# Kernel optimization log

Hardware: AMD Instinct MI355X
Metric: run time of the kernel (lower is better)

Reference implementation:

```python
import jax, jax.numpy as jnp
import numpy as np

E, K, CAP = 64, 8, 512  # num_experts, top_k, per-expert capacity (>= max tokens routed, T*K/E=256 expected)


def setup_inputs() -> dict:
    key = jax.random.key(0)
    ks = jax.random.split(key, 10)
    B, N, D, H, BT, O = 4, 512, 768, 2048, 256, 768
    def w(k, shape, fan_in):
        return jax.random.normal(k, shape, jnp.float32) * np.float32(1.0 / np.sqrt(fan_in))
    return {
        "x": jax.random.normal(ks[0], (B, N, D), jnp.float32),
        "noise": jax.random.normal(ks[1], (B, N, E), jnp.float32),
        "Wr": w(ks[2], (D, E), D), "br": jnp.zeros((E,), jnp.float32),
        "Wn": w(ks[3], (D, E), D), "bn": jnp.zeros((E,), jnp.float32),
        "W1": w(ks[4], (E, D, H), D), "b1": jnp.zeros((E, H), jnp.float32),
        "W2": w(ks[5], (E, H, H), H), "b2": jnp.zeros((E, H), jnp.float32),
        "W3": w(ks[6], (E, H, BT), H), "b3": jnp.zeros((E, BT), jnp.float32),
        "Wo": w(ks[7], (E, BT, O), BT), "bo": jnp.zeros((E, O), jnp.float32),
        "ln_w": jnp.ones((O,), jnp.float32), "ln_b": jnp.zeros((O,), jnp.float32),
    }


def reference(x, noise, Wr, br, Wn, bn, W1, b1, W2, b2, W3, b3, Wo, bo, ln_w, ln_b):
    B, N, D = x.shape
    O = Wo.shape[-1]
    T = B * N
    # --- noisy top-k router ---
    logits = x @ Wr + br                                   # [B,N,E]
    noisy = logits + noise * jax.nn.softplus(x @ Wn + bn)  # [B,N,E]
    topv, topi = jax.lax.top_k(noisy, K)                   # [B,N,K]
    gk = jax.nn.softmax(topv, axis=-1)                     # softmax over top-k == softmax with -inf elsewhere
    fx = x.reshape(T, D)
    fi = topi.reshape(T, K)
    fg = gk.reshape(T, K)
    gate = jnp.zeros((T, E), x.dtype).at[jnp.arange(T)[:, None], fi].set(fg)  # [T,E], zero off top-k
    sel = gate > 0                                         # [T,E] token->expert assignment mask
    # --- capacity-based dispatch (exact: CAP >> max tokens per expert) ---
    selT = sel.T                                           # [E,T]
    idx = jnp.argsort(jnp.logical_not(selT), axis=-1)[:, :CAP]   # [E,CAP] selected tokens first (stable)
    valid = jnp.take_along_axis(selT, idx, axis=1)               # [E,CAP]
    g = jnp.take_along_axis(gate.T, idx, axis=1) * valid          # [E,CAP]
    xin = fx[idx]                                                  # [E,CAP,D]
    gelu = lambda t: jax.nn.gelu(t, approximate=False)
    h = gelu(jnp.einsum('ecd,edh->ech', xin, W1) + b1[:, None, :])
    h = gelu(jnp.einsum('ech,ehf->ecf', h, W2) + b2[:, None, :])
    h = jnp.einsum('ecf,efb->ecb', h, W3) + b3[:, None, :]
    y = jnp.einsum('ecb,ebo->eco', h, Wo) + bo[:, None, :]         # [E,CAP,O]
    y = y * g[:, :, None]                                          # invalid slots weighted by 0
    out = jnp.zeros((T, O), x.dtype).at[idx].add(y)                # scatter-add combine
    # --- LayerNorm ---
    mu = out.mean(-1, keepdims=True)
    var = out.var(-1, keepdims=True)
    out = (out - mu) / jnp.sqrt(var + 1e-5) * ln_w + ln_b
    return out.reshape(B, N, O)
```

## Files before the change

kernel.cpp:

```cpp
#include <hip/hip_runtime.h>
#include <math.h>

#define T_TOK 2048
#define NE 64
#define KTOP 8
#define CAPC 512
#define DIN 768
#define HD 2048
#define BTD 256
#define OD 768

typedef short bf16x8 __attribute__((ext_vector_type(8)));
typedef float f32x4 __attribute__((ext_vector_type(4)));

__device__ __forceinline__ unsigned short f2bf(float f) {
  unsigned u = __float_as_uint(f);
  u += 0x7FFF + ((u >> 16) & 1);
  return (unsigned short)(u >> 16);
}
__device__ __forceinline__ unsigned cvt2(float a, float b) {
  unsigned r;
  asm("v_cvt_pk_bf16_f32 %0, %1, %2" : "=v"(r) : "v"(a), "v"(b));
  return r;
}
__device__ __forceinline__ float gelu_exact(float v) {
  return 0.5f * v * (1.0f + erff(v * 0.7071067811865476f));
}
__device__ __forceinline__ void glds16(unsigned short* lds, const unsigned short* g) {
  __builtin_amdgcn_global_load_lds(
      (const __attribute__((address_space(1))) void*)g,
      (__attribute__((address_space(3))) void*)lds, 16, 0, 0);
}

__global__ __launch_bounds__(256) void cvt_x(const float* __restrict__ x,
                                             unsigned short* __restrict__ xb) {
  int i = blockIdx.x * 256 + threadIdx.x;
  float4 v = ((const float4*)x)[i];
  ushort4 o;
  o.x = f2bf(v.x); o.y = f2bf(v.y); o.z = f2bf(v.z); o.w = f2bf(v.w);
  ((ushort4*)xb)[i] = o;
}

__global__ __launch_bounds__(256) void router_kernel(
    const float* __restrict__ x, const float* __restrict__ noise,
    const float* __restrict__ Wr, const float* __restrict__ br,
    const float* __restrict__ Wn, const float* __restrict__ bn,
    float* __restrict__ gate, int* __restrict__ slotm)
{
  __shared__ float xs[8][DIN];
  __shared__ float wrs[64][NE];
  __shared__ float wns[64][NE];
  const int tid = threadIdx.x;
  const int t0 = blockIdx.x * 8;
  for (int i = tid; i < 8 * (DIN / 4); i += 256) {
    int tt = i / (DIN / 4), c = i % (DIN / 4);
    ((float4*)xs[tt])[c] = ((const float4*)(x + (size_t)(t0 + tt) * DIN))[c];
  }
  const int lane = tid & 63;
  const int wv = tid >> 6;
  const int e = lane;
  const int ta = 2 * wv, tb = ta + 1;
  float ar0 = br[e], ar1 = ar0, an0 = bn[e], an1 = an0;
  for (int d0 = 0; d0 < DIN; d0 += 64) {
    __syncthreads();
    for (int i = tid; i < 64 * NE / 4; i += 256) {
      int dd = i >> 4, c4 = (i & 15) * 4;
      *(float4*)&wrs[dd][c4] = *(const float4*)&Wr[(size_t)(d0 + dd) * NE + c4];
      *(float4*)&wns[dd][c4] = *(const float4*)&Wn[(size_t)(d0 + dd) * NE + c4];
    }
    __syncthreads();
    #pragma unroll 8
    for (int dd = 0; dd < 64; dd++) {
      float wr = wrs[dd][e], wn = wns[dd][e];
      float xa = xs[ta][d0 + dd], xb = xs[tb][d0 + dd];
      ar0 = fmaf(xa, wr, ar0); ar1 = fmaf(xb, wr, ar1);
      an0 = fmaf(xa, wn, an0); an1 = fmaf(xb, wn, an1);
    }
  }
  #pragma unroll
  for (int s = 0; s < 2; s++) {
    int t = t0 + ta + s;
    float lr = s ? ar1 : ar0;
    float lnv = s ? an1 : an0;
    float sp = fmaxf(lnv, 0.f) + log1pf(expf(-fabsf(lnv)));
    float v = lr + noise[(size_t)t * NE + e] * sp;
    float cur = v;
    float topv[KTOP]; int topi[KTOP];
    #pragma unroll
    for (int j = 0; j < KTOP; j++) {
      float bv = cur; int bi = e;
      #pragma unroll
      for (int off = 32; off > 0; off >>= 1) {
        float ov = __shfl_xor(bv, off);
        int   oi = __shfl_xor(bi, off);
        if (ov > bv || (ov == bv && oi < bi)) { bv = ov; bi = oi; }
      }
      topv[j] = bv; topi[j] = bi;
      if (e == bi) cur = -INFINITY;
    }
    float mx = topv[0], se = 0.f, pv[KTOP];
    #pragma unroll
    for (int j = 0; j < KTOP; j++) { pv[j] = expf(topv[j] - mx); se += pv[j]; }
    float inv = 1.f / se;
    float g = 0.f; int sl = -1;
    #pragma unroll
    for (int j = 0; j < KTOP; j++) if (topi[j] == e) { g = pv[j] * inv; sl = j; }
    gate[(size_t)t * NE + e] = (sl >= 0) ? g : 0.f;
    slotm[(size_t)t * NE + e] = sl;
  }
}

__global__ __launch_bounds__(256) void dispatch_kernel(
    const float* __restrict__ gate, const int* __restrict__ slotm,
    int* __restrict__ tok_idx, float* __restrict__ tok_g,
    int* __restrict__ tok_slot, int* __restrict__ counts)
{
  const int e = blockIdx.x;
  const int tid = threadIdx.x;
  __shared__ int wave_off[4];
  int base = 0;
  for (int t0 = 0; t0 < T_TOK; t0 += 256) {
    int t = t0 + tid;
    float g = gate[(size_t)t * NE + e];
    bool p = g > 0.f;
    unsigned long long m = __ballot(p);
    int wv = tid >> 6, lane = tid & 63;
    int pre = __popcll(m & ((1ull << lane) - 1ull));
    if (lane == 0) wave_off[wv] = __popcll(m);
    __syncthreads();
    int off = 0;
    for (int w = 0; w < wv; w++) off += wave_off[w];
    int tot = wave_off[0] + wave_off[1] + wave_off[2] + wave_off[3];
    if (p) {
      int pos = base + off + pre;
      if (pos < CAPC) {
        tok_idx[(size_t)e * CAPC + pos] = t;
        tok_g[(size_t)e * CAPC + pos] = g;
        tok_slot[(size_t)e * CAPC + pos] = slotm[(size_t)t * NE + e];
      }
    }
    base += tot;
    __syncthreads();
  }
  if (tid == 0) counts[e] = min(base, CAPC);
}

template<int KD, int NDT, bool AGATHER, int EPI, int NBN, int BPE>
__global__ __launch_bounds__(512, 1) void moe_gemm320(
    const unsigned short* __restrict__ Abf, const float* __restrict__ Bw,
    const float* __restrict__ bias, void* __restrict__ Outp,
    const int* __restrict__ tok_idx, const float* __restrict__ tok_g,
    const int* __restrict__ tok_slot, const int* __restrict__ counts)
{
  constexpr int NK = KD / 32;
  static_assert(NK % 4 == 0 && NK >= 8, "NK must be multiple of 4");
  const int bid = blockIdx.x;
  const int xcd = bid & 7;
  const int q   = bid >> 3;
  const int e     = (q / BPE) * 8 + xcd;
  const int inner = q % BPE;
  const int n0 = (inner % NBN) * 128;
  const int m0 = (inner / NBN) * 320;
  const int cnt = counts[e];
  if (m0 >= cnt) return;
  const int tid = threadIdx.x;
  const int lane = tid & 63, wave = tid >> 6;

  __shared__ unsigned short AL[3][320][32];
  __shared__ unsigned short BL[2][128][40];

  const bool isB = wave < 4;
  const int  w4  = wave & 3;

  const float* bp = Bw + (size_t)e * KD * NDT + (size_t)(8 * w4) * NDT + n0 + 2 * lane;
  float2 breg[4][8];

  size_t a_off[5];
  if (!isB) {
    #pragma unroll
    for (int qq = 0; qq < 5; qq++) {
      int r  = w4 * 80 + qq * 16 + (lane >> 2);
      int cq = ((lane & 3) - (r >> 1)) & 3;
      size_t rowb;
      if (AGATHER) {
        int gr = min(m0 + r, CAPC - 1);
        int tk = (gr < cnt) ? tok_idx[(size_t)e * CAPC + gr] : 0;
        rowb = (size_t)tk * KD;
      } else {
        int gr = min(m0 + r, CAPC - 1);
        rowb = ((size_t)e * CAPC + gr) * KD;
      }
      a_off[qq] = rowb + 8 * cq;
    }
  }

  auto stageA = [&](int t, unsigned short* Abuf) {
    #pragma unroll
    for (int qq = 0; qq < 5; qq++)
      glds16(Abuf + w4 * 2560 + qq * 512, Abf + a_off[qq] + (size_t)t * 32);
  };
  auto loadB = [&](int t, int p) {
    const float* pb = bp + (size_t)t * 32 * NDT;
    #pragma unroll
    for (int j = 0; j < 8; j++) breg[p][j] = *(const float2*)(pb + (size_t)j * NDT);
  };
  auto writeB = [&](unsigned short* Bbuf, int p) {
    uint4 rx, ry;
    rx.x = cvt2(breg[p][0].x, breg[p][1].x); rx.y = cvt2(breg[p][2].x, breg[p][3].x);
    rx.z = cvt2(breg[p][4].x, breg[p][5].x); rx.w = cvt2(breg[p][6].x, breg[p][7].x);
    ry.x = cvt2(breg[p][0].y, breg[p][1].y); ry.y = cvt2(breg[p][2].y, breg[p][3].y);
    ry.z = cvt2(breg[p][4].y, breg[p][5].y); ry.w = cvt2(breg[p][6].y, breg[p][7].y);
    *(uint4*)(Bbuf + (2 * lane) * 40 + 8 * w4)     = rx;
    *(uint4*)(Bbuf + (2 * lane + 1) * 40 + 8 * w4) = ry;
  };

  const int wm = (wave >> 1) * 80;
  const int wn = (wave & 1) * 64;
  const int li = lane & 15, lg = lane >> 4;
  const int kxa = 8 * ((lg + ((li >> 1) & 3)) & 3);

  f32x4 acc[5][4];
  #pragma unroll
  for (int i = 0; i < 5; i++)
    #pragma unroll
    for (int j = 0; j < 4; j++) acc[i][j] = (f32x4){0.f, 0.f, 0.f, 0.f};

  auto step = [&](const unsigned short* Abuf, const unsigned short* Bbuf) {
    bf16x8 afr[5], bfr[4];
    #pragma unroll
    for (int mi = 0; mi < 5; mi++)
      afr[mi] = *(const bf16x8*)(Abuf + (wm + mi * 16 + li) * 32 + kxa);
    #pragma unroll
    for (int ni = 0; ni < 4; ni++)
      bfr[ni] = *(const bf16x8*)(Bbuf + (wn + ni * 16 + li) * 40 + lg * 8);
    __builtin_amdgcn_s_setprio(1);
    #pragma unroll
    for (int mi = 0; mi < 5; mi++)
      #pragma unroll
      for (int ni = 0; ni < 4; ni++)
        acc[mi][ni] = __builtin_amdgcn_mfma_f32_16x16x32_bf16(afr[mi], bfr[ni], acc[mi][ni], 0, 0, 0);
    __builtin_amdgcn_s_setprio(0);
  };

  unsigned short *A0 = &AL[0][0][0], *A1 = &AL[1][0][0], *A2 = &AL[2][0][0];
  unsigned short *B0 = &BL[0][0][0], *B1 = &BL[1][0][0];

  if (isB) {
    loadB(0, 0); loadB(1, 1); loadB(2, 2);
    asm volatile("s_waitcnt vmcnt(16)" ::: "memory");
    writeB(B0, 0);
    asm volatile("s_waitcnt lgkmcnt(0)" ::: "memory");
  } else {
    stageA(0, A0); stageA(1, A1);
    asm volatile("s_waitcnt vmcnt(5)" ::: "memory");
  }
  __builtin_amdgcn_s_barrier();

  #define SUBITER(p)                                                        \
    do {                                                                    \
      const int jj = jb + (p);                                              \
      if (isB) loadB(min(jj + 3, NK - 1), ((p) + 3) & 3);                   \
      else     stageA(min(jj + 2, NK - 1), A2);                             \
      step(A0, B0);                                                         \
      if (isB) {                                                            \
        asm volatile("s_waitcnt vmcnt(16)" ::: "memory");                   \
        writeB(B1, ((p) + 1) & 3);                                          \
        asm volatile("s_waitcnt lgkmcnt(0)" ::: "memory");                  \
      } else {                                                              \
        asm volatile("s_waitcnt vmcnt(5)" ::: "memory");                    \
      }                                                                     \
      __builtin_amdgcn_s_barrier();                                         \
      unsigned short* ta = A0; A0 = A1; A1 = A2; A2 = ta;                   \
      unsigned short* tb = B0; B0 = B1; B1 = tb;                            \
    } while (0)

  for (int jb = 0; jb < NK; jb += 4) {
    SUBITER(0); SUBITER(1); SUBITER(2); SUBITER(3);
  }
  #undef SUBITER
  asm volatile("s_waitcnt vmcnt(0)" ::: "memory");

  const float* bpb = bias + (size_t)e * NDT;
  #pragma unroll
  for (int mi = 0; mi < 5; mi++) {
    #pragma unroll
    for (int ni = 0; ni < 4; ni++) {
      const int ncol = n0 + wn + ni * 16 + li;
      const float bb = bpb[ncol];
      #pragma unroll
      for (int qq = 0; qq < 4; qq++) {
        const int r = wm + mi * 16 + lg * 4 + qq;
        const int gr = m0 + r;
        if (gr < cnt) {
          float v = acc[mi][ni][qq] + bb;
          if (EPI == 0) v = gelu_exact(v);
          ((unsigned short*)Outp)[((size_t)e * CAPC + gr) * NDT + ncol] = f2bf(v);
        }
      }
    }
  }
}

template<int KD, int ND, bool AGATHER, int EPI, int NBN, int BPE>
__global__ __launch_bounds__(256, 2) void moe_gemm(
    const unsigned short* __restrict__ Abf, const float* __restrict__ Bw,
    const float* __restrict__ bias, void* __restrict__ Outp,
    const int* __restrict__ tok_idx, const float* __restrict__ tok_g,
    const int* __restrict__ tok_slot, const int* __restrict__ counts)
{
  constexpr int NK = KD / 32;
  static_assert(NK % 4 == 0 && NK >= 8, "NK must be multiple of 4");
  const int bid = blockIdx.x;
  const int xcd = bid & 7;
  const int q   = bid >> 3;
  const int e     = (q / BPE) * 8 + xcd;
  const int inner = q % BPE;
  const int n0 = (inner % NBN) * 128;
  const int m0 = (inner / NBN) * 128;
  const int cnt = counts[e];
  if (m0 >= cnt) return;
  const int tid = threadIdx.x;

  __shared__ unsigned short AL[4][128][32];
  __shared__ unsigned short BL[4][128][40];
  __shared__ int   s_tok[128];
  __shared__ float s_g[128];
  __shared__ int   s_slot[128];

  if (EPI == 2 && tid < 128) {
    int gr = m0 + tid;
    if (gr < cnt) {
      s_tok[tid]  = tok_idx[(size_t)e * CAPC + gr];
      s_g[tid]    = tok_g[(size_t)e * CAPC + gr];
      s_slot[tid] = tok_slot[(size_t)e * CAPC + gr];
    }
  }

  const int ar0 = tid >> 2;
  const int ac  = 8 * (((tid & 3) - (tid >> 3)) & 3);
  size_t arow0, arow1;
  if (AGATHER) {
    int g0 = m0 + ar0, g1 = m0 + 64 + ar0;
    int t0i = (g0 < cnt) ? tok_idx[(size_t)e * CAPC + g0] : 0;
    int t1i = (g1 < cnt) ? tok_idx[(size_t)e * CAPC + g1] : 0;
    arow0 = (size_t)t0i * KD; arow1 = (size_t)t1i * KD;
  } else {
    arow0 = ((size_t)e * CAPC + m0 + ar0) * KD;
    arow1 = arow0 + (size_t)64 * KD;
  }
  const unsigned short* ap0 = Abf + arow0 + ac;
  const unsigned short* ap1 = Abf + arow1 + ac;
  const int awb = (tid & 192) * 8;

  const int l = tid & 63, w = tid >> 6;
  const float* bp = Bw + (size_t)e * KD * ND + (size_t)(8 * w) * ND + n0 + 2 * l;

  float2 breg[4][8];

  auto stageA = [&](int t, int s) {
    glds16(&AL[s][0][0] + awb,        ap0 + t * 32);
    glds16(&AL[s][0][0] + 2048 + awb, ap1 + t * 32);
  };
  auto loadB = [&](int t, int p) {
    const float* pb = bp + (size_t)t * 32 * ND;
    #pragma unroll
    for (int j = 0; j < 8; j++) breg[p][j] = *(const float2*)(pb + (size_t)j * ND);
  };
  auto writeB = [&](int s, int p) {
    uint4 rx, ry;
    rx.x = cvt2(breg[p][0].x, breg[p][1].x); rx.y = cvt2(breg[p][2].x, breg[p][3].x);
    rx.z = cvt2(breg[p][4].x, breg[p][5].x); rx.w = cvt2(breg[p][6].x, breg[p][7].x);
    ry.x = cvt2(breg[p][0].y, breg[p][1].y); ry.y = cvt2(breg[p][2].y, breg[p][3].y);
    ry.z = cvt2(breg[p][4].y, breg[p][5].y); ry.w = cvt2(breg[p][6].y, breg[p][7].y);
    *(uint4*)&BL[s][2 * l][8 * w]     = rx;
    *(uint4*)&BL[s][2 * l + 1][8 * w] = ry;
  };

  const int lane = tid & 63, wv = tid >> 6;
  const int wm = (wv >> 1) * 64, wn = (wv & 1) * 64;
  const int li = lane & 15, lg = lane >> 4;
  const int kxa = 8 * ((lg + ((li >> 1) & 3)) & 3);

  f32x4 acc[4][4];
  #pragma unroll
  for (int i = 0; i < 4; i++)
    #pragma unroll
    for (int j = 0; j < 4; j++) acc[i][j] = (f32x4){0.f, 0.f, 0.f, 0.f};

  auto step = [&](int s) {
    bf16x8 afr[4], bfr[4];
    #pragma unroll
    for (int mi = 0; mi < 4; mi++)
      afr[mi] = *(const bf16x8*)&AL[s][wm + mi * 16 + li][kxa];
    #pragma unroll
    for (int ni = 0; ni < 4; ni++)
      bfr[ni] = *(const bf16x8*)&BL[s][wn + ni * 16 + li][lg * 8];
    __builtin_amdgcn_s_setprio(1);
    #pragma unroll
    for (int mi = 0; mi < 4; mi++)
      #pragma unroll
      for (int ni = 0; ni < 4; ni++)
        acc[mi][ni] = __builtin_amdgcn_mfma_f32_16x16x32_bf16(afr[mi], bfr[ni], acc[mi][ni], 0, 0, 0);
    __builtin_amdgcn_s_setprio(0);
  };

  loadB(0, 0);
  stageA(0, 0); loadB(1, 1);
  stageA(1, 1); loadB(2, 2);
  stageA(2, 2); loadB(3, 3);
  asm volatile("s_waitcnt vmcnt(28)" ::: "memory");
  writeB(0, 0);
  asm volatile("s_waitcnt lgkmcnt(0)" ::: "memory");
  __builtin_amdgcn_s_barrier();

  #define SUBITER(p)                                                        \
    do {                                                                    \
      const int jj = jb + (p);                                              \
      stageA(min(jj + 3, NK - 1), ((p) + 3) & 3);                           \
      loadB(min(jj + 4, NK - 1), (p));                                      \
      step(p);                                                              \
      asm volatile("s_waitcnt vmcnt(28)" ::: "memory");                     \
      writeB(((p) + 1) & 3, ((p) + 1) & 3);                                 \
      asm volatile("s_waitcnt lgkmcnt(0)" ::: "memory");                    \
      __builtin_amdgcn_s_barrier();                                         \
    } while (0)

  for (int jb = 0; jb < NK; jb += 4) {
    SUBITER(0); SUBITER(1); SUBITER(2); SUBITER(3);
  }
  #undef SUBITER
  asm volatile("s_waitcnt vmcnt(0)" ::: "memory");

  const float* bpb = bias + (size_t)e * ND;
  #pragma unroll
  for (int mi = 0; mi < 4; mi++) {
    #pragma unroll
    for (int ni = 0; ni < 4; ni++) {
      const int ncol = n0 + wn + ni * 16 + li;
      const float bb = bpb[ncol];
      #pragma unroll
      for (int qq = 0; qq < 4; qq++) {
        const int r = wm + mi * 16 + lg * 4 + qq;
        const int gr = m0 + r;
        if (gr < cnt) {
          float v = acc[mi][ni][qq] + bb;
          if (EPI == 0) {
            v = gelu_exact(v);
            ((unsigned short*)Outp)[((size_t)e * CAPC + gr) * ND + ncol] = f2bf(v);
          } else if (EPI == 1) {
            ((unsigned short*)Outp)[((size_t)e * CAPC + gr) * ND + ncol] = f2bf(v);
          } else {
            ((float*)Outp)[((size_t)s_tok[r] * KTOP + s_slot[r]) * OD + ncol] = v * s_g[r];
          }
        }
      }
    }
  }
}

__global__ __launch_bounds__(256) void combine_ln(
    const float* __restrict__ yd, const float* __restrict__ lw,
    const float* __restrict__ lb, float* __restrict__ out)
{
  const int t = blockIdx.x, tid = threadIdx.x;
  float v[3];
  #pragma unroll
  for (int i = 0; i < 3; i++) {
    const int c = tid + 256 * i;
    float s = 0.f;
    #pragma unroll
    for (int j = 0; j < KTOP; j++) s += yd[((size_t)t * KTOP + j) * OD + c];
    v[i] = s;
  }
  float s1 = v[0] + v[1] + v[2];
  float s2 = v[0] * v[0] + v[1] * v[1] + v[2] * v[2];
  #pragma unroll
  for (int off = 32; off > 0; off >>= 1) {
    s1 += __shfl_xor(s1, off);
    s2 += __shfl_xor(s2, off);
  }
  __shared__ float as1[4], as2[4];
  const int lane = tid & 63, wv = tid >> 6;
  if (lane == 0) { as1[wv] = s1; as2[wv] = s2; }
  __syncthreads();
  s1 = as1[0] + as1[1] + as1[2] + as1[3];
  s2 = as2[0] + as2[1] + as2[2] + as2[3];
  const float mu = s1 * (1.f / OD);
  const float var = s2 * (1.f / OD) - mu * mu;
  const float rstd = rsqrtf(var + 1e-5f);
  #pragma unroll
  for (int i = 0; i < 3; i++) {
    const int c = tid + 256 * i;
    out[(size_t)t * OD + c] = (v[i] - mu) * rstd * lw[c] + lb[c];
  }
}

extern "C" void kernel_launch(void* const* d_in, const int* in_sizes, int n_in,
                              void* d_out, int out_size, void* d_ws, size_t ws_size,
                              hipStream_t stream) {
  const float* x     = (const float*)d_in[0];
  const float* noise = (const float*)d_in[1];
  const float* Wr    = (const float*)d_in[2];
  const float* br    = (const float*)d_in[3];
  const float* Wn    = (const float*)d_in[4];
  const float* bn    = (const float*)d_in[5];
  const float* W1    = (const float*)d_in[6];
  const float* b1    = (const float*)d_in[7];
  const float* W2    = (const float*)d_in[8];
  const float* b2    = (const float*)d_in[9];
  const float* W3    = (const float*)d_in[10];
  const float* b3    = (const float*)d_in[11];
  const float* Wo    = (const float*)d_in[12];
  const float* bo    = (const float*)d_in[13];
  const float* lw    = (const float*)d_in[14];
  const float* lb    = (const float*)d_in[15];
  float* out = (float*)d_out;

  char* ws = (char*)d_ws;
  constexpr size_t OFF_GATE = 0;
  constexpr size_t OFF_SLOT = OFF_GATE + (size_t)T_TOK * NE * 4;
  constexpr size_t OFF_TIDX = OFF_SLOT + (size_t)T_TOK * NE * 4;
  constexpr size_t OFF_TG   = OFF_TIDX + (size_t)NE * CAPC * 4;
  constexpr size_t OFF_TSL  = OFF_TG + (size_t)NE * CAPC * 4;
  constexpr size_t OFF_CNT  = OFF_TSL + (size_t)NE * CAPC * 4;
  constexpr size_t OFF_YD   = ((OFF_CNT + NE * 4) + 255) & ~(size_t)255;
  constexpr size_t SZ_YD    = (size_t)T_TOK * KTOP * OD * 4;
  constexpr size_t OFF_H1   = OFF_YD + SZ_YD;
  constexpr size_t OFF_H2   = OFF_H1 + (size_t)NE * CAPC * HD * 2;
  constexpr size_t OFF_H3   = OFF_H2 + (size_t)NE * CAPC * HD * 2;
  constexpr size_t OFF_XBF  = OFF_H3 + (size_t)NE * CAPC * BTD * 2;

  float* gate = (float*)(ws + OFF_GATE);
  int*   slot = (int*)(ws + OFF_SLOT);
  int*   tidx = (int*)(ws + OFF_TIDX);
  float* tg   = (float*)(ws + OFF_TG);
  int*   tsl  = (int*)(ws + OFF_TSL);
  int*   cnts = (int*)(ws + OFF_CNT);
  float* yd   = (float*)(ws + OFF_YD);
  unsigned short* h1  = (unsigned short*)(ws + OFF_H1);
  unsigned short* h2  = (unsigned short*)(ws + OFF_H2);
  unsigned short* h3  = (unsigned short*)(ws + OFF_H3);
  unsigned short* xbf = (unsigned short*)(ws + OFF_XBF);

  hipMemsetAsync(yd, 0, SZ_YD, stream);
  cvt_x<<<T_TOK * DIN / 4 / 256, 256, 0, stream>>>(x, xbf);
  router_kernel<<<T_TOK / 8, 256, 0, stream>>>(x, noise, Wr, br, Wn, bn, gate, slot);
  dispatch_kernel<<<NE, 256, 0, stream>>>(gate, slot, tidx, tg, tsl, cnts);
  moe_gemm320<DIN, HD, true, 0, 16, 32><<<2048, 512, 0, stream>>>(
      xbf, W1, b1, h1, tidx, tg, tsl, cnts);
  moe_gemm320<HD, HD, false, 0, 16, 32><<<2048, 512, 0, stream>>>(
      h1, W2, b2, h2, tidx, tg, tsl, cnts);
  moe_gemm320<HD, BTD, false, 1, 2, 4><<<256, 512, 0, stream>>>(
      h2, W3, b3, h3, tidx, tg, tsl, cnts);
  moe_gemm<BTD, OD, false, 2, 6, 24><<<1536, 256, 0, stream>>>(
      h3, Wo, bo, yd, tidx, tg, tsl, cnts);
  combine_ln<<<T_TOK, 256, 0, stream>>>(yd, lw, lb, out);
}
```

Before: 845.7 us.

## Split-K the W3 GEMM, swizzle B LDS layout, store combine buffer in bf16

The small W3 GEMM (N=256) launched only 256 blocks, so it now runs as a 2-way split-K writing fp32 partials, and a new h3sum kernel adds the partials and bias and converts to bf16. The B tile in LDS gets an XOR swizzle on its k-chunk to cut bank conflicts in the write and fragment reads. The per-slot output buffer yd is stored as bf16 instead of fp32, halving the memset, scatter and combine traffic at some cost in precision. Split-K adds an extra kernel launch plus an fp32 partial round trip through memory.

Measured after the change: 814.2 us. 3.7% less time.

```diff
diff --git a/kernel.cpp b/kernel.cpp
--- a/kernel.cpp
+++ b/kernel.cpp
@@ -145,22 +145,25 @@
   if (tid == 0) counts[e] = min(base, CAPC);
 }
 
-template<int KD, int NDT, bool AGATHER, int EPI, int NBN, int BPE>
+template<int KD, int NDT, bool AGATHER, int EPI, int NBN, int BPE, int KSPL>
 __global__ __launch_bounds__(512, 1) void moe_gemm320(
     const unsigned short* __restrict__ Abf, const float* __restrict__ Bw,
     const float* __restrict__ bias, void* __restrict__ Outp,
     const int* __restrict__ tok_idx, const float* __restrict__ tok_g,
     const int* __restrict__ tok_slot, const int* __restrict__ counts)
 {
-  constexpr int NK = KD / 32;
-  static_assert(NK % 4 == 0 && NK >= 8, "NK must be multiple of 4");
+  constexpr int NKT = KD / 32;
+  constexpr int NKL = NKT / KSPL;
+  static_assert(NKL % 4 == 0 && NKL >= 8, "NKL must be multiple of 4");
   const int bid = blockIdx.x;
   const int xcd = bid & 7;
   const int q   = bid >> 3;
   const int e     = (q / BPE) * 8 + xcd;
   const int inner = q % BPE;
-  const int n0 = (inner % NBN) * 128;
-  const int m0 = (inner / NBN) * 320;
+  const int n0  = (inner % NBN) * 128;
+  const int ksp = (inner / NBN) % KSPL;
+  const int m0  = (inner / (NBN * KSPL)) * 320;
+  const int kbase = ksp * (KD / KSPL);
   const int cnt = counts[e];
   if (m0 >= cnt) return;
   const int tid = threadIdx.x;
@@ -172,8 +175,9 @@
   const bool isB = wave < 4;
   const int  w4  = wave & 3;
 
-  const float* bp = Bw + (size_t)e * KD * NDT + (size_t)(8 * w4) * NDT + n0 + 2 * lane;
+  const float* bp = Bw + (size_t)e * KD * NDT + (size_t)(kbase + 8 * w4) * NDT + n0 + 2 * lane;
   float2 breg[4][8];
+  const int bxs = 8 * (w4 ^ ((lane >> 2) & 3));
 
   size_t a_off[5];
   if (!isB) {
@@ -182,15 +186,14 @@
       int r  = w4 * 80 + qq * 16 + (lane >> 2);
       int cq = ((lane & 3) - (r >> 1)) & 3;
       size_t rowb;
+      int gr = min(m0 + r, CAPC - 1);
       if (AGATHER) {
-        int gr = min(m0 + r, CAPC - 1);
         int tk = (gr < cnt) ? tok_idx[(size_t)e * CAPC + gr] : 0;
         rowb = (size_t)tk * KD;
       } else {
-        int gr = min(m0 + r, CAPC - 1);
         rowb = ((size_t)e * CAPC + gr) * KD;
       }
-      a_off[qq] = rowb + 8 * cq;
+      a_off[qq] = rowb + kbase + 8 * cq;
     }
   }
 
@@ -210,14 +213,20 @@
     rx.z = cvt2(breg[p][4].x, breg[p][5].x); rx.w = cvt2(breg[p][6].x, breg[p][7].x);
     ry.x = cvt2(breg[p][0].y, breg[p][1].y); ry.y = cvt2(breg[p][2].y, breg[p][3].y);
     ry.z = cvt2(breg[p][4].y, breg[p][5].y); ry.w = cvt2(breg[p][6].y, breg[p][7].y);
-    *(uint4*)(Bbuf + (2 * lane) * 40 + 8 * w4)     = rx;
-    *(uint4*)(Bbuf + (2 * lane + 1) * 40 + 8 * w4) = ry;
+    *(uint4*)(Bbuf + (2 * lane) * 40 + bxs)     = rx;
+    *(uint4*)(Bbuf + (2 * lane + 1) * 40 + bxs) = ry;
   };
 
   const int wm = (wave >> 1) * 80;
   const int wn = (wave & 1) * 64;
   const int li = lane & 15, lg = lane >> 4;
   const int kxa = 8 * ((lg + ((li >> 1) & 3)) & 3);
+  int kxb[4];
+  #pragma unroll
+  for (int ni = 0; ni < 4; ni++) {
+    int row = wn + ni * 16 + li;
+    kxb[ni] = row * 40 + 8 * (lg ^ ((row >> 3) & 3));
+  }
 
   f32x4 acc[5][4];
   #pragma unroll
@@ -232,7 +241,7 @@
       afr[mi] = *(const bf16x8*)(Abuf + (wm + mi * 16 + li) * 32 + kxa);
     #pragma unroll
     for (int ni = 0; ni < 4; ni++)
-      bfr[ni] = *(const bf16x8*)(Bbuf + (wn + ni * 16 + li) * 40 + lg * 8);
+      bfr[ni] = *(const bf16x8*)(Bbuf + kxb[ni]);
     __builtin_amdgcn_s_setprio(1);
     #pragma unroll
     for (int mi = 0; mi < 5; mi++)
@@ -259,8 +268,8 @@
   #define SUBITER(p)                                                        \
     do {                                                                    \
       const int jj = jb + (p);                                              \
-      if (isB) loadB(min(jj + 3, NK - 1), ((p) + 3) & 3);                   \
-      else     stageA(min(jj + 2, NK - 1), A2);                             \
+      if (isB) loadB(min(jj + 3, NKL - 1), ((p) + 3) & 3);                  \
+      else     stageA(min(jj + 2, NKL - 1), A2);                            \
       step(A0, B0);                                                         \
       if (isB) {                                                            \
         asm volatile("s_waitcnt vmcnt(16)" ::: "memory");                   \
@@ -274,7 +283,7 @@
       unsigned short* tb = B0; B0 = B1; B1 = tb;                            \
     } while (0)
 
-  for (int jb = 0; jb < NK; jb += 4) {
+  for (int jb = 0; jb < NKL; jb += 4) {
     SUBITER(0); SUBITER(1); SUBITER(2); SUBITER(3);
   }
   #undef SUBITER
@@ -286,19 +295,41 @@
     #pragma unroll
     for (int ni = 0; ni < 4; ni++) {
       const int ncol = n0 + wn + ni * 16 + li;
-      const float bb = bpb[ncol];
+      const float bb = (EPI == 3) ? 0.f : bpb[ncol];
       #pragma unroll
       for (int qq = 0; qq < 4; qq++) {
         const int r = wm + mi * 16 + lg * 4 + qq;
         const int gr = m0 + r;
         if (gr < cnt) {
           float v = acc[mi][ni][qq] + bb;
-          if (EPI == 0) v = gelu_exact(v);
-          ((unsigned short*)Outp)[((size_t)e * CAPC + gr) * NDT + ncol] = f2bf(v);
+          if (EPI == 0) {
+            v = gelu_exact(v);
+            ((unsigned short*)Outp)[((size_t)e * CAPC + gr) * NDT + ncol] = f2bf(v);
+          } else if (EPI == 1) {
+            ((unsigned short*)Outp)[((size_t)e * CAPC + gr) * NDT + ncol] = f2bf(v);
+          } else {
+            ((float*)Outp)[((size_t)ksp * NE * CAPC + (size_t)e * CAPC + gr) * NDT + ncol] = v;
+          }
         }
       }
     }
   }
+}
+
+__global__ __launch_bounds__(256) void h3sum(const float* __restrict__ p,
+                                             const float* __restrict__ b3,
+                                             unsigned short* __restrict__ h3) {
+  constexpr size_t SEG = (size_t)NE * CAPC * BTD;
+  size_t i = (size_t)blockIdx.x * 1024 + (size_t)threadIdx.x * 4;
+  float4 a = *(const float4*)(p + i);
+  float4 b = *(const float4*)(p + SEG + i);
+  int c = (int)(i % BTD);
+  int e = (int)(i / ((size_t)CAPC * BTD));
+  const float* bb = b3 + (size_t)e * BTD + c;
+  ushort4 o;
+  o.x = f2bf(a.x + b.x + bb[0]); o.y = f2bf(a.y + b.y + bb[1]);
+  o.z = f2bf(a.z + b.z + bb[2]); o.w = f2bf(a.w + b.w + bb[3]);
+  *(ushort4*)(h3 + i) = o;
 }
 
 template<int KD, int ND, bool AGATHER, int EPI, int NBN, int BPE>
@@ -450,7 +481,8 @@
           } else if (EPI == 1) {
             ((unsigned short*)Outp)[((size_t)e * CAPC + gr) * ND + ncol] = f2bf(v);
           } else {
-            ((float*)Outp)[((size_t)s_tok[r] * KTOP + s_slot[r]) * OD + ncol] = v * s_g[r];
+            ((unsigned short*)Outp)[((size_t)s_tok[r] * KTOP + s_slot[r]) * OD + ncol]
+                = f2bf(v * s_g[r]);
           }
         }
       }
@@ -459,7 +491,7 @@
 }
 
 __global__ __launch_bounds__(256) void combine_ln(
-    const float* __restrict__ yd, const float* __restrict__ lw,
+    const unsigned short* __restrict__ yd, const float* __restrict__ lw,
     const float* __restrict__ lb, float* __restrict__ out)
 {
   const int t = blockIdx.x, tid = threadIdx.x;
@@ -469,7 +501,10 @@
     const int c = tid + 256 * i;
     float s = 0.f;
     #pragma unroll
-    for (int j = 0; j < KTOP; j++) s += yd[((size_t)t * KTOP + j) * OD + c];
+    for (int j = 0; j < KTOP; j++) {
+      unsigned u = yd[((size_t)t * KTOP + j) * OD + c];
+      s += __uint_as_float(u << 16);
+    }
     v[i] = s;
   }
   float s1 = v[0] + v[1] + v[2];
@@ -524,11 +559,12 @@
   constexpr size_t OFF_TSL  = OFF_TG + (size_t)NE * CAPC * 4;
   constexpr size_t OFF_CNT  = OFF_TSL + (size_t)NE * CAPC * 4;
   constexpr size_t OFF_YD   = ((OFF_CNT + NE * 4) + 255) & ~(size_t)255;
-  constexpr size_t SZ_YD    = (size_t)T_TOK * KTOP * OD * 4;
-  constexpr size_t OFF_H1   = OFF_YD + SZ_YD;
+  constexpr size_t SZ_YD    = (size_t)T_TOK * KTOP * OD * 2;
+  constexpr size_t OFF_H1   = ((OFF_YD + SZ_YD) + 255) & ~(size_t)255;
   constexpr size_t OFF_H2   = OFF_H1 + (size_t)NE * CAPC * HD * 2;
   constexpr size_t OFF_H3   = OFF_H2 + (size_t)NE * CAPC * HD * 2;
   constexpr size_t OFF_XBF  = OFF_H3 + (size_t)NE * CAPC * BTD * 2;
+  constexpr size_t OFF_H3P  = ((OFF_XBF + (size_t)T_TOK * DIN * 2) + 255) & ~(size_t)255;
 
   float* gate = (float*)(ws + OFF_GATE);
   int*   slot = (int*)(ws + OFF_SLOT);
@@ -536,22 +572,24 @@
   float* tg   = (float*)(ws + OFF_TG);
   int*   tsl  = (int*)(ws + OFF_TSL);
   int*   cnts = (int*)(ws + OFF_CNT);
-  float* yd   = (float*)(ws + OFF_YD);
+  unsigned short* yd  = (unsigned short*)(ws + OFF_YD);
   unsigned short* h1  = (unsigned short*)(ws + OFF_H1);
   unsigned short* h2  = (unsigned short*)(ws + OFF_H2);
   unsigned short* h3  = (unsigned short*)(ws + OFF_H3);
   unsigned short* xbf = (unsigned short*)(ws + OFF_XBF);
+  float* h3p = (float*)(ws + OFF_H3P);
 
   hipMemsetAsync(yd, 0, SZ_YD, stream);
   cvt_x<<<T_TOK * DIN / 4 / 256, 256, 0, stream>>>(x, xbf);
   router_kernel<<<T_TOK / 8, 256, 0, stream>>>(x, noise, Wr, br, Wn, bn, gate, slot);
   dispatch_kernel<<<NE, 256, 0, stream>>>(gate, slot, tidx, tg, tsl, cnts);
-  moe_gemm320<DIN, HD, true, 0, 16, 32><<<2048, 512, 0, stream>>>(
+  moe_gemm320<DIN, HD, true, 0, 16, 32, 1><<<2048, 512, 0, stream>>>(
       xbf, W1, b1, h1, tidx, tg, tsl, cnts);
-  moe_gemm320<HD, HD, false, 0, 16, 32><<<2048, 512, 0, stream>>>(
+  moe_gemm320<HD, HD, false, 0, 16, 32, 1><<<2048, 512, 0, stream>>>(
       h1, W2, b2, h2, tidx, tg, tsl, cnts);
-  moe_gemm320<HD, BTD, false, 1, 2, 4><<<256, 512, 0, stream>>>(
-      h2, W3, b3, h3, tidx, tg, tsl, cnts);
+  moe_gemm320<HD, BTD, false, 3, 2, 8, 2><<<512, 512, 0, stream>>>(
+      h2, W3, b3, h3p, tidx, tg, tsl, cnts);
+  h3sum<<<(NE * CAPC * BTD) / 1024, 256, 0, stream>>>(h3p, b3, h3);
   moe_gemm<BTD, OD, false, 2, 6, 24><<<1536, 256, 0, stream>>>(
       h3, Wo, bo, yd, tidx, tg, tsl, cnts);
   combine_ln<<<T_TOK, 256, 0, stream>>>(yd, lw, lb, out);
```
